# Performance work log

Measured on AMD Instinct MI355X. Metric: run time of the kernel, lower is better.

Reference implementation:

```python
import jax, jax.numpy as jnp
import numpy as np

N, S, C, H, W = 2, 16, 64, 128, 160
NUM_GROUPS = 8


def setup_inputs() -> dict:
    key = jax.random.key(0)
    k1, k2, k3 = jax.random.split(key, 3)
    feat_ref = jax.random.normal(k1, (N, C, H, W), dtype=jnp.float32)
    feat_src = jax.random.normal(k2, (N, C, H, W), dtype=jnp.float32)
    g = jax.random.uniform(k3, (N, S, 2, H, W), dtype=jnp.float32)
    # channel 0 = x in [0, W), channel 1 = y in [0, H) (pixel coordinates)
    scale = jnp.array([W, H], dtype=jnp.float32)[None, None, :, None, None]
    grids = g * scale
    mask = jnp.ones((N, S, H, W), dtype=jnp.float32)
    return {"feat_ref": feat_ref, "feat_src": feat_src, "grids": grids, "mask": mask}


def _warp_bilinear_zeros(feat, gx, gy):
    """Bilinear sample with zeros padding (align_corners=False semantics,
    gx/gy already unnormalized to pixel space).
    feat: [N,C,H,W]; gx, gy: [N,S,H,W].
    Returns warped [N,C,S,H,W] and mask-sum [N,S,H,W] (= grid_sample of ones)."""
    Nb, Cc, Hx, Wx = feat.shape
    x0 = jnp.floor(gx)
    y0 = jnp.floor(gy)
    dx = gx - x0
    dy = gy - y0
    x0i = x0.astype(jnp.int32)
    y0i = y0.astype(jnp.int32)
    corners = [
        (x0i,     y0i,     (1.0 - dx) * (1.0 - dy)),
        (x0i + 1, y0i,     dx * (1.0 - dy)),
        (x0i,     y0i + 1, (1.0 - dx) * dy),
        (x0i + 1, y0i + 1, dx * dy),
    ]
    gather = jax.vmap(lambda img, yy, xx: img[:, yy, xx])  # [C,H,W],[S,H,W]->[C,S,H,W]
    acc = jnp.zeros((Nb, Cc) + gx.shape[1:], dtype=feat.dtype)
    macc = jnp.zeros(gx.shape, dtype=feat.dtype)
    for xi, yi, w in corners:
        valid = ((xi >= 0) & (xi < Wx) & (yi >= 0) & (yi < Hx)).astype(feat.dtype)
        xi_c = jnp.clip(xi, 0, Wx - 1)
        yi_c = jnp.clip(yi, 0, Hx - 1)
        v = gather(feat, yi_c, xi_c)  # [N,C,S,H,W]
        wv = w * valid                # [N,S,H,W]
        acc = acc + v * wv[:, None]
        macc = macc + wv
    return acc, macc


def reference(feat_ref, feat_src, grids, mask):
    Nb, Cc, Hx, Wx = feat_src.shape
    Sn = grids.shape[1]
    gc = Cc // NUM_GROUPS
    # torch code normalizes pixel coords to [-1,1], grid_sample (align_corners=False)
    # unnormalizes back: net effect is sampling at (coord - 0.5)
    xg, yg = grids[:, :, 0], grids[:, :, 1]          # [N,S,H,W]
    xn = 2.0 * xg / Wx - 1.0
    yn = 2.0 * yg / Hx - 1.0
    gx = ((xn + 1.0) * Wx - 1.0) / 2.0
    gy = ((yn + 1.0) * Hx - 1.0) / 2.0
    warped, m = _warp_bilinear_zeros(feat_src, gx, gy)  # [N,C,S,H,W], [N,S,H,W]
    # warping mask: grid_sample of ones with zeros padding, then binarize
    warping_mask = jnp.where(m < 0.9999, 0.0, 1.0).astype(feat_src.dtype)
    # groupwise correlation: sum over channels within each group
    warped_g = warped.reshape(Nb, NUM_GROUPS, gc, Sn, Hx, Wx)
    ref_g = feat_ref.reshape(Nb, NUM_GROUPS, gc, Hx, Wx)
    corr = jnp.einsum('ngcshw,ngchw->ngshw', warped_g, ref_g)  # [N,G,S,H,W]
    corr = corr * warping_mask[:, None]
    corr = corr * mask[:, None]
    warping_mask = warping_mask * mask
    return corr, warping_mask
```

## Files before the change

kernel.cpp:

```cpp
#include <hip/hip_runtime.h>
#include <hip/hip_bf16.h>

#define Nn 2
#define Ss 16
#define Cc 64
#define Hh 128
#define Ww 160
#define Gg 8
#define HW (Hh * Ww)
#define NPS (Nn * Ss * HW)

struct Prep {
  float4 w;
  int4 o;
};

__global__ __launch_bounds__(256) void transpose2_nchw_nhwc(
    const float* __restrict__ ref, const float* __restrict__ srcf,
    float* __restrict__ ref_t, float* __restrict__ src_t) {
  const float* sp = blockIdx.y ? srcf : ref;
  float* dp = blockIdx.y ? src_t : ref_t;
  const int WT = 32;
  __shared__ float tile[Cc][WT + 1];
  int b = blockIdx.x;
  int wt = b % (Ww / WT);
  int h  = (b / (Ww / WT)) % Hh;
  int n  = b / ((Ww / WT) * Hh);
  int w0 = wt * WT;
  int tid = threadIdx.x;
#pragma unroll
  for (int i = 0; i < (Cc * WT) / 256; ++i) {
    int idx = tid + i * 256;
    int c  = idx >> 5;
    int ww = idx & 31;
    tile[c][ww] = sp[((n * Cc + c) * Hh + h) * Ww + w0 + ww];
  }
  __syncthreads();
#pragma unroll
  for (int i = 0; i < (Cc * WT) / 256; ++i) {
    int idx = tid + i * 256;
    int ww = idx >> 6;
    int c  = idx & 63;
    dp[((n * Hh + h) * Ww + w0 + ww) * Cc + c] = tile[c][ww];
  }
}

__global__ __launch_bounds__(256) void prep_kernel(
    const float* __restrict__ grids, const float* __restrict__ mask,
    Prep* __restrict__ prep, float* __restrict__ wmask) {
  int hw = blockIdx.x * 256 + threadIdx.x;
  int ns = blockIdx.y;
  int idx = ns * HW + hw;

  float xg = grids[(ns * 2) * HW + hw];
  float yg = grids[(ns * 2 + 1) * HW + hw];
  float mk = mask[idx];

  float xn = 2.0f * xg / (float)Ww - 1.0f;
  float yn = 2.0f * yg / (float)Hh - 1.0f;
  float gx = ((xn + 1.0f) * (float)Ww - 1.0f) * 0.5f;
  float gy = ((yn + 1.0f) * (float)Hh - 1.0f) * 0.5f;

  float x0f = floorf(gx), y0f = floorf(gy);
  float dx = gx - x0f, dy = gy - y0f;
  int x0 = (int)x0f, y0 = (int)y0f;
  int x1 = x0 + 1, y1 = y0 + 1;

  float vx0 = (x0 >= 0 && x0 < Ww) ? 1.f : 0.f;
  float vx1 = (x1 >= 0 && x1 < Ww) ? 1.f : 0.f;
  float vy0 = (y0 >= 0 && y0 < Hh) ? 1.f : 0.f;
  float vy1 = (y1 >= 0 && y1 < Hh) ? 1.f : 0.f;

  float w00 = (1.f - dx) * (1.f - dy) * vx0 * vy0;
  float w10 = dx * (1.f - dy) * vx1 * vy0;
  float w01 = (1.f - dx) * dy * vx0 * vy1;
  float w11 = dx * dy * vx1 * vy1;

  float m  = w00 + w10 + w01 + w11;
  float wm = (m < 0.9999f) ? 0.f : 1.f;
  float scale = wm * mk;

  int x0c = min(max(x0, 0), Ww - 1), x1c = min(max(x1, 0), Ww - 1);
  int y0c = min(max(y0, 0), Hh - 1), y1c = min(max(y1, 0), Hh - 1);

  Prep p;
  p.w = make_float4(w00 * scale, w10 * scale, w01 * scale, w11 * scale);
  p.o = make_int4(y0c * Ww + x0c, y0c * Ww + x1c, y1c * Ww + x0c, y1c * Ww + x1c);
  prep[idx] = p;
  wmask[idx] = scale;
}

__global__ __launch_bounds__(256) void corr_main(
    const float* __restrict__ ref_t, const float* __restrict__ src_t,
    const Prep* __restrict__ prep, float* __restrict__ corr) {
  int nwg = gridDim.x;
  int q = nwg >> 3;
  int b = blockIdx.x;
  int swz = (b & 7) * q + (b >> 3);
  int wid  = threadIdx.x >> 6;
  int lane = threadIdx.x & 63;
  int hw = swz * 4 + wid;
  int n  = blockIdx.y;

  float rv = ref_t[(n * HW + hw) * Cc + lane];
  const float* srcn = src_t + (size_t)n * HW * Cc;
  const Prep* pp = prep + (size_t)(n * Ss) * HW + hw;
  int cbase = ((n * Gg + (lane >> 3)) * Ss) * HW + hw;

  float4 w = pp->w;
  int4   o = pp->o;
#pragma unroll
  for (int s = 0; s < Ss; ++s) {
    float4 wN; int4 oN;
    if (s + 1 < Ss) {
      wN = pp[(s + 1) * HW].w;
      oN = pp[(s + 1) * HW].o;
    }
    float v00 = srcn[o.x * Cc + lane];
    float v10 = srcn[o.y * Cc + lane];
    float v01 = srcn[o.z * Cc + lane];
    float v11 = srcn[o.w * Cc + lane];
    float acc = w.x * v00;
    acc = fmaf(w.y, v10, acc);
    acc = fmaf(w.z, v01, acc);
    acc = fmaf(w.w, v11, acc);
    float p = acc * rv;
    p += __shfl_xor(p, 1);
    p += __shfl_xor(p, 2);
    p += __shfl_xor(p, 4);
    if ((lane & 7) == 0) corr[cbase + s * HW] = p;
    w = wN; o = oN;
  }
}

template <bool NHWC>
__global__ __launch_bounds__(256) void corr_kernel(
    const float* __restrict__ ref, const float* __restrict__ src,
    const float* __restrict__ grids, const float* __restrict__ mask,
    float* __restrict__ corr, float* __restrict__ wmask) {
  int gw   = blockIdx.x * 4 + (threadIdx.x >> 6);
  int lane = threadIdx.x & 63;
  int w  = gw % Ww;
  int hn = gw / Ww;
  int h  = hn % Hh;
  int n  = hn / Hh;

  float rv = NHWC ? ref[((n * Hh + h) * Ww + w) * Cc + lane]
                  : ref[((n * Cc + lane) * Hh + h) * Ww + w];

#pragma unroll 4
  for (int s = 0; s < Ss; ++s) {
    int gbase = (((n * Ss + s) * 2) * Hh + h) * Ww + w;
    float xg = grids[gbase];
    float yg = grids[gbase + HW];
    float mk = mask[((n * Ss + s) * Hh + h) * Ww + w];

    float xn = 2.0f * xg / (float)Ww - 1.0f;
    float yn = 2.0f * yg / (float)Hh - 1.0f;
    float gx = ((xn + 1.0f) * (float)Ww - 1.0f) * 0.5f;
    float gy = ((yn + 1.0f) * (float)Hh - 1.0f) * 0.5f;

    float x0f = floorf(gx), y0f = floorf(gy);
    float dx = gx - x0f, dy = gy - y0f;
    int x0 = (int)x0f, y0 = (int)y0f;
    int x1 = x0 + 1, y1 = y0 + 1;

    float vx0 = (x0 >= 0 && x0 < Ww) ? 1.f : 0.f;
    float vx1 = (x1 >= 0 && x1 < Ww) ? 1.f : 0.f;
    float vy0 = (y0 >= 0 && y0 < Hh) ? 1.f : 0.f;
    float vy1 = (y1 >= 0 && y1 < Hh) ? 1.f : 0.f;

    float w00 = (1.f - dx) * (1.f - dy) * vx0 * vy0;
    float w10 = dx * (1.f - dy) * vx1 * vy0;
    float w01 = (1.f - dx) * dy * vx0 * vy1;
    float w11 = dx * dy * vx1 * vy1;

    float m  = w00 + w10 + w01 + w11;
    float wm = (m < 0.9999f) ? 0.f : 1.f;
    float scale = wm * mk;

    float res = 0.f;
    if (scale != 0.f) {
      int x0c = min(max(x0, 0), Ww - 1), x1c = min(max(x1, 0), Ww - 1);
      int y0c = min(max(y0, 0), Hh - 1), y1c = min(max(y1, 0), Hh - 1);
      float v00, v10, v01, v11;
      if (NHWC) {
        v00 = src[((n * Hh + y0c) * Ww + x0c) * Cc + lane];
        v10 = src[((n * Hh + y0c) * Ww + x1c) * Cc + lane];
        v01 = src[((n * Hh + y1c) * Ww + x0c) * Cc + lane];
        v11 = src[((n * Hh + y1c) * Ww + x1c) * Cc + lane];
      } else {
        const float* sp2 = src + (size_t)(n * Cc + lane) * HW;
        v00 = sp2[y0c * Ww + x0c];
        v10 = sp2[y0c * Ww + x1c];
        v01 = sp2[y1c * Ww + x0c];
        v11 = sp2[y1c * Ww + x1c];
      }
      float acc = w00 * v00 + w10 * v10 + w01 * v01 + w11 * v11;
      float p = acc * rv * scale;
      p += __shfl_xor(p, 1);
      p += __shfl_xor(p, 2);
      p += __shfl_xor(p, 4);
      res = p;
    }
    if ((lane & 7) == 0) {
      int g = lane >> 3;
      corr[((((n * Gg + g) * Ss + s) * Hh + h) * Ww) + w] = res;
    }
    if (lane == 0) wmask[((n * Ss + s) * Hh + h) * Ww + w] = scale;
  }
}

extern "C" void kernel_launch(void* const* d_in, const int* in_sizes, int n_in,
                              void* d_out, int out_size, void* d_ws, size_t ws_size,
                              hipStream_t stream) {
  const float* feat_ref = (const float*)d_in[0];
  const float* feat_src = (const float*)d_in[1];
  const float* grids    = (const float*)d_in[2];
  const float* mask     = (const float*)d_in[3];

  float* corr  = (float*)d_out;
  float* wmask = corr + (size_t)Nn * Gg * Ss * HW;

  const size_t bytes_t   = (size_t)Nn * Cc * HW * sizeof(float);
  const size_t prep_off  = 2 * bytes_t;
  const size_t prep_size = (size_t)NPS * sizeof(Prep);

  if (ws_size >= prep_off + prep_size) {
    float* ref_t = (float*)d_ws;
    float* src_t = ref_t + (size_t)Nn * Cc * HW;
    Prep*  prep  = (Prep*)((char*)d_ws + prep_off);
    prep_kernel<<<dim3(HW / 256, Nn * Ss), 256, 0, stream>>>(grids, mask, prep, wmask);
    transpose2_nchw_nhwc<<<dim3(Nn * Hh * (Ww / 32), 2), 256, 0, stream>>>(
        feat_ref, feat_src, ref_t, src_t);
    corr_main<<<dim3(HW / 4, Nn), 256, 0, stream>>>(ref_t, src_t, prep, corr);
  } else if (ws_size >= 2 * bytes_t) {
    float* ref_t = (float*)d_ws;
    float* src_t = ref_t + (size_t)Nn * Cc * HW;
    transpose2_nchw_nhwc<<<dim3(Nn * Hh * (Ww / 32), 2), 256, 0, stream>>>(
        feat_ref, feat_src, ref_t, src_t);
    corr_kernel<true><<<(Nn * HW) / 4, 256, 0, stream>>>(ref_t, src_t, grids, mask, corr, wmask);
  } else {
    corr_kernel<false><<<(Nn * HW) / 4, 256, 0, stream>>>(feat_ref, feat_src, grids, mask, corr, wmask);
  }
}
```

Baseline: 170.2 us.

## Split bilinear corners across lane quarters with float4 loads in corr_main

Reworks the correlation kernel so each 16-lane quarter of a wavefront handles one bilinear corner. Each lane loads a float4 covering four channels instead of one scalar per corner. The prep buffer is re-laid out as interleaved (weight, offset) pairs per corner, and the loop now prefetches the gathered source vector one step ahead and the weight/offset two steps ahead. The aim is fewer, wider memory instructions and more latency hiding for the gathers. In exchange, the group reduction needs cross-quarter shuffles (xor 16, 32, 1) and each lane holds more live registers.

```diff
diff --git a/kernel.cpp b/kernel.cpp
--- a/kernel.cpp
+++ b/kernel.cpp
@@ -10,10 +10,7 @@
 #define HW (Hh * Ww)
 #define NPS (Nn * Ss * HW)
 
-struct Prep {
-  float4 w;
-  int4 o;
-};
+struct WO { float w; int o; };
 
 __global__ __launch_bounds__(256) void transpose2_nchw_nhwc(
     const float* __restrict__ ref, const float* __restrict__ srcf,
@@ -47,7 +44,7 @@
 
 __global__ __launch_bounds__(256) void prep_kernel(
     const float* __restrict__ grids, const float* __restrict__ mask,
-    Prep* __restrict__ prep, float* __restrict__ wmask) {
+    WO* __restrict__ prep, float* __restrict__ wmask) {
   int hw = blockIdx.x * 256 + threadIdx.x;
   int ns = blockIdx.y;
   int idx = ns * HW + hw;
@@ -83,53 +80,60 @@
   int x0c = min(max(x0, 0), Ww - 1), x1c = min(max(x1, 0), Ww - 1);
   int y0c = min(max(y0, 0), Hh - 1), y1c = min(max(y1, 0), Hh - 1);
 
-  Prep p;
-  p.w = make_float4(w00 * scale, w10 * scale, w01 * scale, w11 * scale);
-  p.o = make_int4(y0c * Ww + x0c, y0c * Ww + x1c, y1c * Ww + x0c, y1c * Ww + x1c);
-  prep[idx] = p;
+  int4 a, b;
+  a.x = __float_as_int(w00 * scale); a.y = y0c * Ww + x0c;
+  a.z = __float_as_int(w10 * scale); a.w = y0c * Ww + x1c;
+  b.x = __float_as_int(w01 * scale); b.y = y1c * Ww + x0c;
+  b.z = __float_as_int(w11 * scale); b.w = y1c * Ww + x1c;
+  int4* op = (int4*)(prep + (size_t)idx * 4);
+  op[0] = a;
+  op[1] = b;
   wmask[idx] = scale;
 }
 
 __global__ __launch_bounds__(256) void corr_main(
     const float* __restrict__ ref_t, const float* __restrict__ src_t,
-    const Prep* __restrict__ prep, float* __restrict__ corr) {
+    const WO* __restrict__ prep, float* __restrict__ corr) {
   int nwg = gridDim.x;
-  int q = nwg >> 3;
-  int b = blockIdx.x;
-  int swz = (b & 7) * q + (b >> 3);
+  int q8 = nwg >> 3;
+  int bb = blockIdx.x;
+  int swz = (bb & 7) * q8 + (bb >> 3);
   int wid  = threadIdx.x >> 6;
   int lane = threadIdx.x & 63;
+  int k = lane & 15;
   int hw = swz * 4 + wid;
   int n  = blockIdx.y;
 
-  float rv = ref_t[(n * HW + hw) * Cc + lane];
+  float4 rv = *(const float4*)(ref_t + ((size_t)(n * HW) + hw) * Cc + 4 * k);
   const float* srcn = src_t + (size_t)n * HW * Cc;
-  const Prep* pp = prep + (size_t)(n * Ss) * HW + hw;
-  int cbase = ((n * Gg + (lane >> 3)) * Ss) * HW + hw;
-
-  float4 w = pp->w;
-  int4   o = pp->o;
+  const WO* pp = prep + ((size_t)(n * Ss) * HW + hw) * 4 + (lane >> 4);
+  const int PSTRIDE = HW * 4;
+
+  int cbase = ((n * Gg + (k >> 1)) * Ss) * HW + hw;
+
+  WO wo0 = pp[0];
+  float4 v0 = *(const float4*)(srcn + ((size_t)wo0.o << 6) + (k << 2));
+  WO wo1 = pp[PSTRIDE];
+
 #pragma unroll
   for (int s = 0; s < Ss; ++s) {
-    float4 wN; int4 oN;
-    if (s + 1 < Ss) {
-      wN = pp[(s + 1) * HW].w;
-      oN = pp[(s + 1) * HW].o;
-    }
-    float v00 = srcn[o.x * Cc + lane];
-    float v10 = srcn[o.y * Cc + lane];
-    float v01 = srcn[o.z * Cc + lane];
-    float v11 = srcn[o.w * Cc + lane];
-    float acc = w.x * v00;
-    acc = fmaf(w.y, v10, acc);
-    acc = fmaf(w.z, v01, acc);
-    acc = fmaf(w.w, v11, acc);
-    float p = acc * rv;
+    WO wo2; float4 v1;
+    if (s + 2 < Ss) wo2 = pp[(s + 2) * PSTRIDE];
+    if (s + 1 < Ss) v1 = *(const float4*)(srcn + ((size_t)wo1.o << 6) + (k << 2));
+
+    float d = v0.x * rv.x;
+    d = fmaf(v0.y, rv.y, d);
+    d = fmaf(v0.z, rv.z, d);
+    d = fmaf(v0.w, rv.w, d);
+    float p = d * wo0.w;
+
+    p += __shfl_xor(p, 16);
+    p += __shfl_xor(p, 32);
     p += __shfl_xor(p, 1);
-    p += __shfl_xor(p, 2);
-    p += __shfl_xor(p, 4);
-    if ((lane & 7) == 0) corr[cbase + s * HW] = p;
-    w = wN; o = oN;
+
+    if (lane < 16 && (lane & 1) == 0) corr[cbase + s * HW] = p;
+
+    wo0 = wo1; wo1 = wo2; v0 = v1;
   }
 }
 
@@ -224,12 +228,12 @@
 
   const size_t bytes_t   = (size_t)Nn * Cc * HW * sizeof(float);
   const size_t prep_off  = 2 * bytes_t;
-  const size_t prep_size = (size_t)NPS * sizeof(Prep);
+  const size_t prep_size = (size_t)NPS * 4 * sizeof(WO);
 
   if (ws_size >= prep_off + prep_size) {
     float* ref_t = (float*)d_ws;
     float* src_t = ref_t + (size_t)Nn * Cc * HW;
-    Prep*  prep  = (Prep*)((char*)d_ws + prep_off);
+    WO*    prep  = (WO*)((char*)d_ws + prep_off);
     prep_kernel<<<dim3(HW / 256, Nn * Ss), 256, 0, stream>>>(grids, mask, prep, wmask);
     transpose2_nchw_nhwc<<<dim3(Nn * Hh * (Ww / 32), 2), 256, 0, stream>>>(
         feat_ref, feat_src, ref_t, src_t);
```

Result: faster. 154.0 us (-9.5%).
